# Kernel tuning notes

Measured on AMD Instinct MI355X. Metric: run time of the kernel, lower is better.

## Reference

```python
import jax, jax.numpy as jnp
import numpy as np

D_MODEL = 1024
N_HEADS = 16
D_K = D_MODEL // N_HEADS
B, S = 2, 2048


def setup_inputs() -> dict:
    key = jax.random.key(0)
    ks = jax.random.split(key, 12)
    scale = 1.0 / np.sqrt(D_MODEL)
    inp = {
        "query": jax.random.normal(ks[0], (B, S, D_MODEL), jnp.float32),
        "key": jax.random.normal(ks[1], (B, S, D_MODEL), jnp.float32),
        "value": jax.random.normal(ks[2], (B, S, D_MODEL), jnp.float32),
        "mask": jnp.tril(jnp.ones((S, S), dtype=bool))[None, None],  # (1,1,S,S) causal
        "W_q": jax.random.normal(ks[3], (D_MODEL, D_MODEL), jnp.float32) * scale,
        "b_q": jnp.zeros((D_MODEL,), jnp.float32),
        "W_k": jax.random.normal(ks[4], (D_MODEL, D_MODEL), jnp.float32) * scale,
        "b_k": jnp.zeros((D_MODEL,), jnp.float32),
        "W_v": jax.random.normal(ks[5], (D_MODEL, D_MODEL), jnp.float32) * scale,
        "b_v": jnp.zeros((D_MODEL,), jnp.float32),
        "W_o": jax.random.normal(ks[6], (D_MODEL, D_MODEL), jnp.float32) * scale,
        "b_o": jnp.zeros((D_MODEL,), jnp.float32),
    }
    return inp


def reference(query, key, value, mask, W_q, b_q, W_k, b_k, W_v, b_v, W_o, b_o):
    b = query.shape[0]
    # Linear projections (torch Linear: x @ W.T + b), split into heads -> (b,h,s,d_k)
    def proj(x, W, bias):
        y = x @ W.T + bias
        return y.reshape(b, -1, N_HEADS, D_K).transpose(0, 2, 1, 3)

    q = proj(query, W_q, b_q)
    k = proj(key, W_k, b_k)
    v = proj(value, W_v, b_v)

    # scores: (b,h,sq,sk)
    scores = jnp.einsum("bhqd,bhkd->bhqk", q, k) / jnp.sqrt(jnp.float32(D_K)).astype(q.dtype)
    scores = jnp.where(mask, scores, jnp.finfo(scores.dtype).min)
    attn = jax.nn.softmax(scores, axis=-1)
    out = jnp.einsum("bhqk,bhkd->bhqd", attn, v)  # (b,h,sq,d_k)
    out = out.transpose(0, 2, 1, 3).reshape(b, -1, D_MODEL)
    return out @ W_o.T + b_o
```

## Files before the change

kernel.cpp:

```cpp
#include <hip/hip_runtime.h>
#include <hip/hip_bf16.h>
#include <stdint.h>

#define D_MODEL 1024
#define NH 16
#define DK 64
#define BB 2
#define SS 2048
#define MROWS (BB*SS)

typedef __attribute__((ext_vector_type(8))) short bf16x8;
typedef __attribute__((ext_vector_type(4))) float f32x4;

__device__ __forceinline__ short to_bf16(float f) {
  __hip_bfloat16 h = __float2bfloat16(f);
  union { __hip_bfloat16 b; short s; } u; u.b = h; return u.s;
}

__device__ __forceinline__ f32x4 mfma16(bf16x8 a, bf16x8 b, f32x4 c) {
  return __builtin_amdgcn_mfma_f32_16x16x32_bf16(a, b, c, 0, 0, 0);
}

__device__ __forceinline__ void gload_lds16(const void* g, void* l) {
  __builtin_amdgcn_global_load_lds(
      (const __attribute__((address_space(1))) unsigned int*)g,
      (__attribute__((address_space(3))) unsigned int*)l,
      16, 0, 0);
}

__device__ __forceinline__ float max3f(float a, float b, float c) {
  return fmaxf(fmaxf(a, b), c);
}

__global__ __launch_bounds__(256) void cvt3(const float* __restrict__ a,
                                            const float* __restrict__ b,
                                            const float* __restrict__ c,
                                            short* __restrict__ oa,
                                            short* __restrict__ ob,
                                            short* __restrict__ oc) {
  const int z = blockIdx.z;
  const float* x = z == 0 ? a : z == 1 ? b : c;
  short* y = z == 0 ? oa : z == 1 ? ob : oc;
  const int i = (blockIdx.x * 256 + threadIdx.x) * 4;
  const float4 v = *(const float4*)(x + i);
  short4 o;
  o.x = to_bf16(v.x); o.y = to_bf16(v.y); o.z = to_bf16(v.z); o.w = to_bf16(v.w);
  *(short4*)(y + i) = o;
}

__global__ __launch_bounds__(256) void cvt4(const float* __restrict__ a,
                                            const float* __restrict__ b,
                                            const float* __restrict__ c,
                                            const float* __restrict__ d,
                                            short* __restrict__ oa,
                                            short* __restrict__ ob,
                                            short* __restrict__ oc,
                                            short* __restrict__ od) {
  const int z = blockIdx.z;
  const float* x = z == 0 ? a : z == 1 ? b : z == 2 ? c : d;
  short* y = z == 0 ? oa : z == 1 ? ob : z == 2 ? oc : od;
  const int i = (blockIdx.x * 256 + threadIdx.x) * 4;
  const float4 v = *(const float4*)(x + i);
  short4 o;
  o.x = to_bf16(v.x); o.y = to_bf16(v.y); o.z = to_bf16(v.z); o.w = to_bf16(v.w);
  *(short4*)(y + i) = o;
}

__global__ __launch_bounds__(256) void gemm_qkv(const short* __restrict__ Xq,
                                                const short* __restrict__ Xk,
                                                const short* __restrict__ Xv,
                                                const short* __restrict__ Wq,
                                                const short* __restrict__ Wk,
                                                const short* __restrict__ Wv,
                                                const float* __restrict__ bq,
                                                const float* __restrict__ bk,
                                                const float* __restrict__ bv,
                                                short* __restrict__ Qh,
                                                short* __restrict__ Kh,
                                                short* __restrict__ VT) {
  constexpr int K = 1024;
  __shared__ short As[128 * 64];
  __shared__ short Bs[128 * 64];
  const int z = blockIdx.z;
  const short* A    = z == 0 ? Xq : z == 1 ? Xk : Xv;
  const short* Wt   = z == 0 ? Wq : z == 1 ? Wk : Wv;
  const float* bias = z == 0 ? bq : z == 1 ? bk : bv;

  const int tid = threadIdx.x;
  const int w = tid >> 6, lane = tid & 63;
  const int m0 = blockIdx.x * 128, n0 = blockIdx.y * 128;
  const int wm = w >> 1, wn = w & 1;
  const int fr = lane & 15, fg = lane >> 4;
  const int srow = tid >> 3, scol = (tid & 7) * 8;

  f32x4 acc[4][4] = {};

  for (int k0 = 0; k0 < K; k0 += 64) {
    __syncthreads();
#pragma unroll
    for (int i = 0; i < 4; ++i) {
      const int row = i * 32 + srow;
      gload_lds16(A  + (size_t)(m0 + row) * K + k0 + scol, As + row * 64 + scol);
      gload_lds16(Wt + (size_t)(n0 + row) * K + k0 + scol, Bs + row * 64 + scol);
    }
    asm volatile("s_waitcnt vmcnt(0)" ::: "memory");
    __syncthreads();

    bf16x8 af[4][2], bfr[4][2];
#pragma unroll
    for (int i = 0; i < 4; ++i)
#pragma unroll
      for (int hh = 0; hh < 2; ++hh) {
        af[i][hh]  = *(const bf16x8*)(As + (wm * 64 + i * 16 + fr) * 64 + hh * 32 + fg * 8);
        bfr[i][hh] = *(const bf16x8*)(Bs + (wn * 64 + i * 16 + fr) * 64 + hh * 32 + fg * 8);
      }
    __builtin_amdgcn_s_setprio(1);
#pragma unroll
    for (int mi = 0; mi < 4; ++mi)
#pragma unroll
      for (int ni = 0; ni < 4; ++ni) {
        acc[mi][ni] = mfma16(af[mi][0], bfr[ni][0], acc[mi][ni]);
        acc[mi][ni] = mfma16(af[mi][1], bfr[ni][1], acc[mi][ni]);
      }
    __builtin_amdgcn_s_setprio(0);
  }

  const float scale = (z == 0) ? 0.18033688011112042f : 1.0f;
#pragma unroll
  for (int mi = 0; mi < 4; ++mi)
#pragma unroll
    for (int ni = 0; ni < 4; ++ni) {
      const int col = n0 + wn * 64 + ni * 16 + fr;
      const float bval = bias[col];
      const int h = col >> 6, d = col & 63;
#pragma unroll
      for (int r = 0; r < 4; ++r) {
        const int row = m0 + wm * 64 + mi * 16 + fg * 4 + r;
        const float val = (acc[mi][ni][r] + bval) * scale;
        const int b = row >> 11, s = row & (SS - 1);
        if (z < 2) {
          short* dst = (z == 0) ? Qh : Kh;
          dst[((size_t)(b * NH + h) * SS + s) * DK + d] = to_bf16(val);
        } else {
          VT[((size_t)(b * NH + h) * DK + d) * SS + s] = to_bf16(val);
        }
      }
    }
}

__global__ __launch_bounds__(256) void gemm_out(const short* __restrict__ A,
                                                const short* __restrict__ Wt,
                                                const float* __restrict__ bias,
                                                float* __restrict__ Y) {
  constexpr int K = 1024;
  __shared__ short As[128 * 64];
  __shared__ short Bs[64 * 64];
  const int tid = threadIdx.x;
  const int w = tid >> 6, lane = tid & 63;
  const int m0 = blockIdx.x * 128, n0 = blockIdx.y * 64;
  const int wm = w >> 1, wn = w & 1;
  const int fr = lane & 15, fg = lane >> 4;
  const int srow = tid >> 3, scol = (tid & 7) * 8;

  f32x4 acc[4][2] = {};

  for (int k0 = 0; k0 < K; k0 += 64) {
    __syncthreads();
#pragma unroll
    for (int i = 0; i < 4; ++i) {
      const int row = i * 32 + srow;
      gload_lds16(A + (size_t)(m0 + row) * K + k0 + scol, As + row * 64 + scol);
    }
#pragma unroll
    for (int i = 0; i < 2; ++i) {
      const int row = i * 32 + srow;
      gload_lds16(Wt + (size_t)(n0 + row) * K + k0 + scol, Bs + row * 64 + scol);
    }
    asm volatile("s_waitcnt vmcnt(0)" ::: "memory");
    __syncthreads();

    bf16x8 af[4][2], bfr[2][2];
#pragma unroll
    for (int i = 0; i < 4; ++i)
#pragma unroll
      for (int hh = 0; hh < 2; ++hh)
        af[i][hh] = *(const bf16x8*)(As + (wm * 64 + i * 16 + fr) * 64 + hh * 32 + fg * 8);
#pragma unroll
    for (int i = 0; i < 2; ++i)
#pragma unroll
      for (int hh = 0; hh < 2; ++hh)
        bfr[i][hh] = *(const bf16x8*)(Bs + (wn * 32 + i * 16 + fr) * 64 + hh * 32 + fg * 8);
    __builtin_amdgcn_s_setprio(1);
#pragma unroll
    for (int mi = 0; mi < 4; ++mi)
#pragma unroll
      for (int ni = 0; ni < 2; ++ni) {
        acc[mi][ni] = mfma16(af[mi][0], bfr[ni][0], acc[mi][ni]);
        acc[mi][ni] = mfma16(af[mi][1], bfr[ni][1], acc[mi][ni]);
      }
    __builtin_amdgcn_s_setprio(0);
  }

#pragma unroll
  for (int mi = 0; mi < 4; ++mi)
#pragma unroll
    for (int ni = 0; ni < 2; ++ni) {
      const int col = n0 + wn * 32 + ni * 16 + fr;
      const float bval = bias[col];
#pragma unroll
      for (int r = 0; r < 4; ++r) {
        const int row = m0 + wm * 64 + mi * 16 + fg * 4 + r;
        Y[(size_t)row * D_MODEL + col] = acc[mi][ni][r] + bval;
      }
    }
}

__global__ __launch_bounds__(256) void attn_kernel(const short* __restrict__ Qh,
                                                   const short* __restrict__ Kh,
                                                   const short* __restrict__ VT,
                                                   short* __restrict__ AO) {
  __shared__ short Ks[3][64 * 64];
  __shared__ short Vs[3][64 * 64];
  __shared__ short P_lds[4][16 * 64];

  const int tid = threadIdx.x, w = tid >> 6, lane = tid & 63;
  const int fr = lane & 15, fg = lane >> 4;
  const int kr = fg * 4;
  const int swz = (fr & 7) << 4;

  const int bid = blockIdx.x;
  const int lid = ((bid & 7) << 6) | (bid >> 3);
  const int bh = lid >> 4;
  const int j = lid & 15;
  const int b = bh >> 4, h = bh & 15;

  const short* Qp = Qh + (size_t)bh * SS * DK;
  const short* Kp = Kh + (size_t)bh * SS * DK;
  const short* Vp = VT + (size_t)bh * DK * SS;

  const int sc_c = tid & 7;
  const int sc_r = tid >> 3;

  const int T0 = j + 1;

  bf16x8 qf[2];
#pragma unroll
  for (int hh = 0; hh < 2; ++hh)
    qf[hh] = *(const bf16x8*)(Qp + (size_t)(j * 64 + w * 16 + fr) * DK + hh * 32 + fg * 8);

  const short onev = (fr == 0) ? (short)0x3F80 : (short)0;
  const bf16x8 af4 = {onev, onev, onev, onev, onev, onev, onev, onev};

  f32x4 o[5] = {};
  float m_run = -1e30f;
  f32x4 stA[4], stB[4];

#define KK0(g) ((((g) < T0) ? (g) : ((g) - T0)) * 64)
#define STAGE_KV(buf, kk0)                                                    \
  do {                                                                        \
    _Pragma("unroll") for (int p = 0; p < 2; ++p) {                           \
      const int row = p * 32 + sc_r;                                          \
      const int sc = sc_c ^ (row & 7);                                        \
      gload_lds16(Kp + (size_t)((kk0) + row) * DK + sc * 8,                   \
                  &Ks[buf][row * 64 + sc_c * 8]);                             \
      gload_lds16(Vp + (size_t)row * SS + (kk0) + sc * 8,                     \
                  &Vs[buf][row * 64 + sc_c * 8]);                             \
    }                                                                         \
  } while (0)

  auto softmax_pv = [&](int bufPrev) {
    float p0 = max3f(stB[0][0], stB[0][1], stB[0][2]);
    float p1 = max3f(stB[0][3], stB[1][0], stB[1][1]);
    float p2 = max3f(stB[1][2], stB[1][3], stB[2][0]);
    float p3 = max3f(stB[2][1], stB[2][2], stB[2][3]);
    float p4 = max3f(stB[3][0], stB[3][1], stB[3][2]);
    float pmax = fmaxf(max3f(p0, p1, p2), max3f(p3, p4, stB[3][3]));
    pmax = fmaxf(pmax, __shfl_xor(pmax, 16));
    pmax = fmaxf(pmax, __shfl_xor(pmax, 32));

    if (!__all(pmax <= m_run + 11.0f)) {
      const float mn = fmaxf(m_run, pmax);
      const float al = __builtin_amdgcn_exp2f(m_run - mn);
      m_run = mn;
#pragma unroll
      for (int t = 0; t < 5; ++t)
#pragma unroll
        for (int r = 0; r < 4; ++r) o[t][r] *= al;
    }

    char* base = (char*)P_lds[w];
#pragma unroll
    for (int kt = 0; kt < 4; ++kt) {
      short4 sv;
      sv.x = to_bf16(__builtin_amdgcn_exp2f(stB[kt][0] - m_run));
      sv.y = to_bf16(__builtin_amdgcn_exp2f(stB[kt][1] - m_run));
      sv.z = to_bf16(__builtin_amdgcn_exp2f(stB[kt][2] - m_run));
      sv.w = to_bf16(__builtin_amdgcn_exp2f(stB[kt][3] - m_run));
      *(short4*)(base + ((fr * 128 + kt * 32 + fg * 8) ^ swz)) = sv;
    }
    asm volatile("s_waitcnt lgkmcnt(0)" ::: "memory");

    const char* VsB = (const char*)Vs[bufPrev];
    __builtin_amdgcn_s_setprio(1);
#pragma unroll
    for (int c = 0; c < 2; ++c) {
      const bf16x8 pf = *(const bf16x8*)((const char*)P_lds[w] +
                                         ((fr * 128 + c * 64 + fg * 16) ^ swz));
#pragma unroll
      for (int t = 0; t < 4; ++t) {
        const bf16x8 vfb = *(const bf16x8*)(VsB + (t * 16 + fr) * 128 +
                                            ((c * 64 + fg * 16) ^ swz));
        o[t] = mfma16(vfb, pf, o[t]);
      }
      o[4] = mfma16(af4, pf, o[4]);
    }
    __builtin_amdgcn_s_setprio(0);
  };

  auto store_o = [&](int qbase) {
    const float l = __shfl(o[4][0], fr);
    const float inv = 1.0f / l;
    const int s = qbase + w * 16 + fr;
#pragma unroll
    for (int t = 0; t < 4; ++t) {
      short4 ov = {to_bf16(o[t][0] * inv), to_bf16(o[t][1] * inv),
                   to_bf16(o[t][2] * inv), to_bf16(o[t][3] * inv)};
      *(short4*)(AO + (size_t)(b * SS + s) * D_MODEL + h * 64 + t * 16 + kr) = ov;
    }
  };

  STAGE_KV(0, 0);
  STAGE_KV(1, KK0(1));
  asm volatile("s_waitcnt vmcnt(0)" ::: "memory");
  __syncthreads();

  for (int g = 0; g < 33; ++g) {
    if (g == T0) {
#pragma unroll
      for (int hh = 0; hh < 2; ++hh)
        qf[hh] = *(const bf16x8*)(Qp + (size_t)((31 - j) * 64 + w * 16 + fr) * DK + hh * 32 + fg * 8);
    }

    {
      const char* KsB = (const char*)Ks[g % 3];
      __builtin_amdgcn_s_setprio(1);
#pragma unroll
      for (int kt = 0; kt < 4; ++kt) {
        const bf16x8 k0f = *(const bf16x8*)(KsB + (kt * 16 + fr) * 128 + ((fg * 16) ^ swz));
        const bf16x8 k1f = *(const bf16x8*)(KsB + (kt * 16 + fr) * 128 + ((64 + fg * 16) ^ swz));
        f32x4 z = {};
        z = mfma16(k0f, qf[0], z);
        z = mfma16(k1f, qf[1], z);
        stA[kt] = z;
      }
      __builtin_amdgcn_s_setprio(0);
    }
    if (g == T0 - 1 || g == 32) {
#pragma unroll
      for (int kt = 0; kt < 4; ++kt)
#pragma unroll
        for (int r = 0; r < 4; ++r)
          if (kt * 16 + kr + r > w * 16 + fr) stA[kt][r] = -1e30f;
    }

    if (g > 0) {
      softmax_pv((g - 1) % 3);
      if (g == T0) {
        store_o(j * 64);
#pragma unroll
        for (int t = 0; t < 5; ++t)
#pragma unroll
          for (int r = 0; r < 4; ++r) o[t][r] = 0.f;
        m_run = -1e30f;
      }
    }

#pragma unroll
    for (int kt = 0; kt < 4; ++kt) stB[kt] = stA[kt];

    asm volatile("s_waitcnt vmcnt(0)" ::: "memory");
    __syncthreads();
    if (g + 2 <= 32) STAGE_KV((g + 2) % 3, KK0(g + 2));
  }

  softmax_pv(32 % 3);
  store_o((31 - j) * 64);
#undef STAGE_KV
#undef KK0
}

extern "C" void kernel_launch(void* const* d_in, const int* in_sizes, int n_in,
                              void* d_out, int out_size, void* d_ws, size_t ws_size,
                              hipStream_t stream) {
  const float* q  = (const float*)d_in[0];
  const float* k  = (const float*)d_in[1];
  const float* v  = (const float*)d_in[2];
  const float* Wq = (const float*)d_in[4];
  const float* bq = (const float*)d_in[5];
  const float* Wk = (const float*)d_in[6];
  const float* bk = (const float*)d_in[7];
  const float* Wv = (const float*)d_in[8];
  const float* bv = (const float*)d_in[9];
  const float* Wo = (const float*)d_in[10];
  const float* bo = (const float*)d_in[11];

  char* ws = (char*)d_ws;
  const size_t MB = 1u << 20;
  short* Xq = (short*)(ws + 0 * MB);
  short* Xk = (short*)(ws + 8 * MB);
  short* Xv = (short*)(ws + 16 * MB);
  short* Bq = (short*)(ws + 24 * MB);
  short* Bk = (short*)(ws + 26 * MB);
  short* Bv = (short*)(ws + 28 * MB);
  short* Bo = (short*)(ws + 30 * MB);
  short* Qh = (short*)(ws + 32 * MB);
  short* Kh = (short*)(ws + 40 * MB);
  short* VT = (short*)(ws + 48 * MB);
  short* AO = (short*)(ws + 56 * MB);

  cvt3<<<dim3(MROWS * D_MODEL / 1024, 1, 3), 256, 0, stream>>>(q, k, v, Xq, Xk, Xv);
  cvt4<<<dim3(D_MODEL * D_MODEL / 1024, 1, 4), 256, 0, stream>>>(Wq, Wk, Wv, Wo, Bq, Bk, Bv, Bo);

  gemm_qkv<<<dim3(MROWS / 128, D_MODEL / 128, 3), 256, 0, stream>>>(
      Xq, Xk, Xv, Bq, Bk, Bv, bq, bk, bv, Qh, Kh, VT);

  attn_kernel<<<dim3(512), 256, 0, stream>>>(Qh, Kh, VT, AO);

  gemm_out<<<dim3(MROWS / 128, D_MODEL / 64), 256, 0, stream>>>(AO, Bo, bo, (float*)d_out);
}
```

Baseline: 123.7 us.

## Double-buffer LDS tiles in QKV and output projection GEMMs

Both projection GEMMs now use two LDS buffers with a K-step of 32 instead of a single buffer with a K-step of 64. The next tile's global-to-LDS loads are issued before the MFMAs on the current tile, so memory latency overlaps compute. In exchange there are twice as many iterations and barriers, each with half as many MFMAs, and LDS rows are 64 bytes, which may change bank-conflict patterns.

Measured after the change: 123.2 us. About the same (-0.4%).

```diff
diff --git a/kernel.cpp b/kernel.cpp
--- a/kernel.cpp
+++ b/kernel.cpp
@@ -78,9 +78,9 @@
                                                 short* __restrict__ Qh,
                                                 short* __restrict__ Kh,
                                                 short* __restrict__ VT) {
-  constexpr int K = 1024;
-  __shared__ short As[128 * 64];
-  __shared__ short Bs[128 * 64];
+  constexpr int K = 1024, NSTEP = K / 32;
+  __shared__ short As[2][128 * 32];
+  __shared__ short Bs[2][128 * 32];
   const int z = blockIdx.z;
   const short* A    = z == 0 ? Xq : z == 1 ? Xk : Xv;
   const short* Wt   = z == 0 ? Wq : z == 1 ? Wk : Wv;
@@ -91,39 +91,47 @@
   const int m0 = blockIdx.x * 128, n0 = blockIdx.y * 128;
   const int wm = w >> 1, wn = w & 1;
   const int fr = lane & 15, fg = lane >> 4;
-  const int srow = tid >> 3, scol = (tid & 7) * 8;
+  const int srow = tid >> 2, scol = (tid & 3) * 8;
 
   f32x4 acc[4][4] = {};
 
-  for (int k0 = 0; k0 < K; k0 += 64) {
-    __syncthreads();
+#define QKV_STAGE(buf, k0)                                                    \
+  do {                                                                        \
+    _Pragma("unroll") for (int i = 0; i < 2; ++i) {                           \
+      const int row = i * 64 + srow;                                          \
+      gload_lds16(A  + (size_t)(m0 + row) * K + (k0) + scol,                  \
+                  &As[buf][row * 32 + scol]);                                 \
+      gload_lds16(Wt + (size_t)(n0 + row) * K + (k0) + scol,                  \
+                  &Bs[buf][row * 32 + scol]);                                 \
+    }                                                                         \
+  } while (0)
+
+  QKV_STAGE(0, 0);
+  asm volatile("s_waitcnt vmcnt(0)" ::: "memory");
+  __syncthreads();
+
+  for (int t = 0; t < NSTEP; ++t) {
+    const int cur = t & 1;
+    if (t + 1 < NSTEP) QKV_STAGE(cur ^ 1, (t + 1) * 32);
+
+    bf16x8 af[4], bfr[4];
 #pragma unroll
     for (int i = 0; i < 4; ++i) {
-      const int row = i * 32 + srow;
-      gload_lds16(A  + (size_t)(m0 + row) * K + k0 + scol, As + row * 64 + scol);
-      gload_lds16(Wt + (size_t)(n0 + row) * K + k0 + scol, Bs + row * 64 + scol);
-    }
+      af[i]  = *(const bf16x8*)(&As[cur][(wm * 64 + i * 16 + fr) * 32 + fg * 8]);
+      bfr[i] = *(const bf16x8*)(&Bs[cur][(wn * 64 + i * 16 + fr) * 32 + fg * 8]);
+    }
+    __builtin_amdgcn_s_setprio(1);
+#pragma unroll
+    for (int mi = 0; mi < 4; ++mi)
+#pragma unroll
+      for (int ni = 0; ni < 4; ++ni)
+        acc[mi][ni] = mfma16(af[mi], bfr[ni], acc[mi][ni]);
+    __builtin_amdgcn_s_setprio(0);
+
     asm volatile("s_waitcnt vmcnt(0)" ::: "memory");
     __syncthreads();
-
-    bf16x8 af[4][2], bfr[4][2];
-#pragma unroll
-    for (int i = 0; i < 4; ++i)
-#pragma unroll
-      for (int hh = 0; hh < 2; ++hh) {
-        af[i][hh]  = *(const bf16x8*)(As + (wm * 64 + i * 16 + fr) * 64 + hh * 32 + fg * 8);
-        bfr[i][hh] = *(const bf16x8*)(Bs + (wn * 64 + i * 16 + fr) * 64 + hh * 32 + fg * 8);
-      }
-    __builtin_amdgcn_s_setprio(1);
-#pragma unroll
-    for (int mi = 0; mi < 4; ++mi)
-#pragma unroll
-      for (int ni = 0; ni < 4; ++ni) {
-        acc[mi][ni] = mfma16(af[mi][0], bfr[ni][0], acc[mi][ni]);
-        acc[mi][ni] = mfma16(af[mi][1], bfr[ni][1], acc[mi][ni]);
-      }
-    __builtin_amdgcn_s_setprio(0);
   }
+#undef QKV_STAGE
 
   const float scale = (z == 0) ? 0.18033688011112042f : 1.0f;
 #pragma unroll
@@ -152,54 +160,57 @@
                                                 const short* __restrict__ Wt,
                                                 const float* __restrict__ bias,
                                                 float* __restrict__ Y) {
-  constexpr int K = 1024;
-  __shared__ short As[128 * 64];
-  __shared__ short Bs[64 * 64];
+  constexpr int K = 1024, NSTEP = K / 32;
+  __shared__ short As[2][128 * 32];
+  __shared__ short Bs[2][64 * 32];
   const int tid = threadIdx.x;
   const int w = tid >> 6, lane = tid & 63;
   const int m0 = blockIdx.x * 128, n0 = blockIdx.y * 64;
   const int wm = w >> 1, wn = w & 1;
   const int fr = lane & 15, fg = lane >> 4;
-  const int srow = tid >> 3, scol = (tid & 7) * 8;
+  const int srow = tid >> 2, scol = (tid & 3) * 8;
 
   f32x4 acc[4][2] = {};
 
-  for (int k0 = 0; k0 < K; k0 += 64) {
-    __syncthreads();
-#pragma unroll
-    for (int i = 0; i < 4; ++i) {
-      const int row = i * 32 + srow;
-      gload_lds16(A + (size_t)(m0 + row) * K + k0 + scol, As + row * 64 + scol);
-    }
-#pragma unroll
-    for (int i = 0; i < 2; ++i) {
-      const int row = i * 32 + srow;
-      gload_lds16(Wt + (size_t)(n0 + row) * K + k0 + scol, Bs + row * 64 + scol);
-    }
+#define OUT_STAGE(buf, k0)                                                    \
+  do {                                                                        \
+    _Pragma("unroll") for (int i = 0; i < 2; ++i) {                           \
+      const int row = i * 64 + srow;                                          \
+      gload_lds16(A + (size_t)(m0 + row) * K + (k0) + scol,                   \
+                  &As[buf][row * 32 + scol]);                                 \
+    }                                                                         \
+    if (srow < 64)                                                            \
+      gload_lds16(Wt + (size_t)(n0 + srow) * K + (k0) + scol,                 \
+                  &Bs[buf][srow * 32 + scol]);                                \
+  } while (0)
+
+  OUT_STAGE(0, 0);
+  asm volatile("s_waitcnt vmcnt(0)" ::: "memory");
+  __syncthreads();
+
+  for (int t = 0; t < NSTEP; ++t) {
+    const int cur = t & 1;
+    if (t + 1 < NSTEP) OUT_STAGE(cur ^ 1, (t + 1) * 32);
+
+    bf16x8 af[4], bfr[2];
+#pragma unroll
+    for (int i = 0; i < 4; ++i)
+      af[i] = *(const bf16x8*)(&As[cur][(wm * 64 + i * 16 + fr) * 32 + fg * 8]);
+#pragma unroll
+    for (int i = 0; i < 2; ++i)
+      bfr[i] = *(const bf16x8*)(&Bs[cur][(wn * 32 + i * 16 + fr) * 32 + fg * 8]);
+    __builtin_amdgcn_s_setprio(1);
+#pragma unroll
+    for (int mi = 0; mi < 4; ++mi)
+#pragma unroll
+      for (int ni = 0; ni < 2; ++ni)
+        acc[mi][ni] = mfma16(af[mi], bfr[ni], acc[mi][ni]);
+    __builtin_amdgcn_s_setprio(0);
+
     asm volatile("s_waitcnt vmcnt(0)" ::: "memory");
     __syncthreads();
-
-    bf16x8 af[4][2], bfr[2][2];
-#pragma unroll
-    for (int i = 0; i < 4; ++i)
-#pragma unroll
-      for (int hh = 0; hh < 2; ++hh)
-        af[i][hh] = *(const bf16x8*)(As + (wm * 64 + i * 16 + fr) * 64 + hh * 32 + fg * 8);
-#pragma unroll
-    for (int i = 0; i < 2; ++i)
-#pragma unroll
-      for (int hh = 0; hh < 2; ++hh)
-        bfr[i][hh] = *(const bf16x8*)(Bs + (wn * 32 + i * 16 + fr) * 64 + hh * 32 + fg * 8);
-    __builtin_amdgcn_s_setprio(1);
-#pragma unroll
-    for (int mi = 0; mi < 4; ++mi)
-#pragma unroll
-      for (int ni = 0; ni < 2; ++ni) {
-        acc[mi][ni] = mfma16(af[mi][0], bfr[ni][0], acc[mi][ni]);
-        acc[mi][ni] = mfma16(af[mi][1], bfr[ni][1], acc[mi][ni]);
-      }
-    __builtin_amdgcn_s_setprio(0);
   }
+#undef OUT_STAGE
 
 #pragma unroll
   for (int mi = 0; mi < 4; ++mi)
```
